# Kernel tuning notes

Hardware: AMD Instinct MI355X
Metric: run time of the kernel (lower is better)

Reference implementation:

```python
import jax, jax.numpy as jnp
import numpy as np

B, N, F = 8, 1024, 256
OUT, REL = 256, 16
NADJ = 7  # ((2 relations + consecutive) * 2 for backward) + self link


def setup_inputs() -> dict:
    key = jax.random.key(0)
    k0, k1, k2, k3, k4 = jax.random.split(key, 5)
    features = jax.random.normal(k0, (B, N, F), dtype=jnp.float32)
    A1 = jax.random.uniform(k1, (B, N, N), dtype=jnp.float32)
    A2 = jax.random.uniform(k2, (B, N, N), dtype=jnp.float32)
    # learned params: one (F+REL, OUT) weight per adjacency matrix, edge embeddings init 'ones', bias (N, OUT)
    W = jax.random.normal(k3, (NADJ, F + REL, OUT), dtype=jnp.float32) * 0.05
    W_edges = jnp.ones((NADJ, REL), dtype=jnp.float32)
    b = jax.random.uniform(k4, (N, OUT), dtype=jnp.float32, minval=-0.05, maxval=0.05)
    return {"features": features, "A1": A1, "A2": A2, "W": W, "W_edges": W_edges, "b": b}


def reference(features, A1, A2, W, W_edges, b):
    # eye = A[0] * zeros(N) + eye(N)  -> batch-broadcast identity [B,N,N]
    eye = jnp.zeros_like(A1) + jnp.eye(N, dtype=A1.dtype)
    # original rolls along axis 0 (batch) of the broadcast identity (faithful replication)
    shifted = jnp.roll(eye, 1, axis=0)
    A_fwd = [A1, A2, shifted]                      # relations + consecutive link
    A_list = A_fwd + [jnp.swapaxes(a, 1, 2) for a in A_fwd]  # backward links
    A_list.append(eye)                             # self links
    A = jnp.stack(A_list, axis=0)                  # [R,B,N,N]

    # concat(features, tile(W_edges[r])) @ W[r] == features @ W[r][:F] + W_edges[r] @ W[r][F:]
    HW = jnp.einsum('bnf,rfo->rbno', features, W[:, :F]) \
         + jnp.einsum('rd,rdo->ro', W_edges, W[:, F:])[:, None, None, :]  # [R,B,N,OUT]
    AHW = jnp.einsum('rbnm,rbmo->rbno', A, HW)     # batched adjacency matmul
    out = jnp.max(AHW, axis=0) + b                 # max-aggregate over relations, add bias
    return out                                     # activation = linear
```

## Files before the change

### kernel.cpp

```cpp
#include <hip/hip_runtime.h>
#include <hip/hip_bf16.h>

#define B_ 8
#define N_ 1024
#define F_ 256
#define OUT_ 256
#define REL_ 16
#define NADJ_ 7

typedef __attribute__((ext_vector_type(8))) _Float16 f16x8;
typedef __attribute__((ext_vector_type(4))) float f32x4;

__device__ __forceinline__ void gll16(const _Float16* g, _Float16* l) {
    __builtin_amdgcn_global_load_lds(
        (const __attribute__((address_space(1))) void*)g,
        (__attribute__((address_space(3))) void*)l, 16, 0, 0);
}

__constant__ const int c_perm[7] = {0, 1, 3, 4, 2, 5, 6};

__global__ __launch_bounds__(256) void convprep_kernel(const float* __restrict__ A1,
                                                       const float* __restrict__ A2,
                                                       const float* __restrict__ W,
                                                       const float* __restrict__ We,
                                                       const float* __restrict__ feat,
                                                       _Float16* __restrict__ Af,
                                                       float* __restrict__ cb,
                                                       _Float16* __restrict__ WTp,
                                                       _Float16* __restrict__ Fe) {
    __shared__ _Float16 T[4096];
    int bid = blockIdx.x, t = threadIdx.x;
    if (bid < 4096) {
        int z = bid >> 8, s = z >> 3, b = z & 7;
        const float* src = (s ? A2 : A1) + (size_t)b * N_ * N_;
        int k0 = (bid & 15) * 64, n0 = ((bid >> 4) & 15) * 64;
        int r = t >> 2, cs = (t & 3) * 16;
        const float* sp = src + (size_t)(k0 + r) * N_ + n0 + cs;
        _Float16 v[16];
#pragma unroll
        for (int j = 0; j < 16; j += 4) {
            float4 f = *(const float4*)(sp + j);
            v[j] = (_Float16)f.x; v[j + 1] = (_Float16)f.y;
            v[j + 2] = (_Float16)f.z; v[j + 3] = (_Float16)f.w;
        }
        const size_t slab = (size_t)8 * N_ * N_;
        {
            _Float16* dst = Af + (size_t)s * slab + (size_t)b * N_ * N_ + (size_t)(k0 + r) * N_ + n0 + cs;
            f16x8 p0 = {v[0], v[1], v[2], v[3], v[4], v[5], v[6], v[7]};
            f16x8 p1 = {v[8], v[9], v[10], v[11], v[12], v[13], v[14], v[15]};
            *(f16x8*)dst = p0;
            *(f16x8*)(dst + 8) = p1;
        }
#pragma unroll
        for (int j = 0; j < 16; ++j) {
            int n = cs + j;
            int sw = ((n ^ (n >> 3)) & 7) << 3;
            T[n * 64 + (r ^ sw)] = v[j];
        }
        __syncthreads();
        {
            int n = t >> 2, i2 = (t & 3) * 16;
            int sw = ((n ^ (n >> 3)) & 7) << 3;
            f16x8 q0 = *(const f16x8*)&T[n * 64 + (i2 ^ sw)];
            f16x8 q1 = *(const f16x8*)&T[n * 64 + ((i2 + 8) ^ sw)];
            _Float16* dt = Af + (size_t)(2 + s) * slab + (size_t)b * N_ * N_ + (size_t)(n0 + n) * N_ + k0 + i2;
            *(f16x8*)dt = q0;
            *(f16x8*)(dt + 8) = q1;
        }
    } else if (bid < 4103) {
        int idx = (bid - 4096) * 256 + t;
        int j = idx / OUT_, o = idx % OUT_;
        int r = c_perm[j];
        const float* Wr = W + (size_t)r * (F_ + REL_) * OUT_;
        float s = 0.f;
#pragma unroll
        for (int d = 0; d < REL_; ++d) s += We[r * REL_ + d] * Wr[(F_ + d) * OUT_ + o];
        cb[idx] = s;
    } else if (bid < 5895) {
        int idx = (bid - 4103) * 256 + t;
        int j = idx >> 16, rem = idx & 65535, o = rem >> 8, f = rem & 255;
        int r = c_perm[j];
        WTp[idx] = (_Float16)W[((size_t)r * (F_ + REL_) + f) * OUT_ + o];
    } else {
        int i = (bid - 5895) * 256 + t;
        size_t base = (size_t)i * 8;
        float4 a = *(const float4*)(feat + base);
        float4 b = *(const float4*)(feat + base + 4);
        f16x8 v = {(_Float16)a.x, (_Float16)a.y, (_Float16)a.z, (_Float16)a.w,
                   (_Float16)b.x, (_Float16)b.y, (_Float16)b.z, (_Float16)b.w};
        *(f16x8*)(Fe + base) = v;
    }
}

__global__ __launch_bounds__(256) void hw7_kernel(const _Float16* __restrict__ Fe,
                                                  const _Float16* __restrict__ WTp,
                                                  const float* __restrict__ cb,
                                                  _Float16* __restrict__ HWT,
                                                  _Float16* __restrict__ HWN) {
    __shared__ _Float16 As[128 * 32];
    __shared__ _Float16 Bs[128 * 32];
    const int z = blockIdx.z, bx = blockIdx.x, by = blockIdx.y;
    const bool tr = (z < 4);
    const _Float16* A  = tr ? (WTp + (size_t)z * 65536) : Fe;
    const _Float16* Bt = tr ? Fe : (WTp + (size_t)z * 65536);
    const int m0 = (tr ? by : bx) * 128;
    const int n0 = (tr ? bx : by) * 128;
    const int tid = threadIdx.x;
    const int wave = tid >> 6, lane = tid & 63, lm = lane & 15, q = lane >> 4;
    const int wr = (wave >> 1) * 64, wc = (wave & 1) * 64;
    const int srow = tid >> 2, sk = (tid & 3) * 8;
    const _Float16* ga0 = A + (size_t)(m0 + srow) * F_ + sk;
    const _Float16* ga1 = ga0 + (size_t)64 * F_;
    const _Float16* gb0 = Bt + (size_t)(n0 + srow) * F_ + sk;
    const _Float16* gb1 = gb0 + (size_t)64 * F_;
    _Float16* la0 = As + tid * 8;
    _Float16* la1 = As + 2048 + tid * 8;
    _Float16* lb0 = Bs + tid * 8;
    _Float16* lb1 = Bs + 2048 + tid * 8;

    f32x4 acc[4][4] = {};
    for (int k0 = 0; k0 < F_; k0 += 32) {
        gll16(ga0 + k0, la0);
        gll16(ga1 + k0, la1);
        gll16(gb0 + k0, lb0);
        gll16(gb1 + k0, lb1);
        __syncthreads();
        f16x8 af[4], bf[4];
#pragma unroll
        for (int i = 0; i < 4; ++i) af[i] = *(const f16x8*)(As + (wr + i * 16 + lm) * 32 + q * 8);
#pragma unroll
        for (int j = 0; j < 4; ++j) bf[j] = *(const f16x8*)(Bs + (wc + j * 16 + lm) * 32 + q * 8);
#pragma unroll
        for (int i = 0; i < 4; ++i)
#pragma unroll
            for (int j = 0; j < 4; ++j)
                acc[i][j] = __builtin_amdgcn_mfma_f32_16x16x32_f16(af[i], bf[j], acc[i][j], 0, 0, 0);
        __syncthreads();
    }
    const float* cbz = cb + (size_t)z * 256;
    if (tr) {
        _Float16* C = HWT + (size_t)z * ((size_t)256 * 8192);
#pragma unroll
        for (int i = 0; i < 4; ++i)
#pragma unroll
            for (int j = 0; j < 4; ++j)
#pragma unroll
                for (int g = 0; g < 4; ++g) {
                    int row = wr + i * 16 + q * 4 + g;
                    int col = wc + j * 16 + lm;
                    float v = acc[i][j][g] + cbz[m0 + row];
                    C[(size_t)(m0 + row) * 8192 + (n0 + col)] = (_Float16)v;
                }
    } else {
        _Float16* C = HWN + (size_t)(z - 4) * ((size_t)8192 * 256);
#pragma unroll
        for (int i = 0; i < 4; ++i)
#pragma unroll
            for (int j = 0; j < 4; ++j)
#pragma unroll
                for (int g = 0; g < 4; ++g) {
                    int row = wr + i * 16 + q * 4 + g;
                    int col = wc + j * 16 + lm;
                    float v = acc[i][j][g] + cbz[n0 + col];
                    C[(size_t)(m0 + row) * 256 + (n0 + col)] = (_Float16)v;
                }
    }
}

__global__ __launch_bounds__(256) void p2_kernel(const _Float16* __restrict__ Af,
                                                 const _Float16* __restrict__ HWT,
                                                 _Float16* __restrict__ AHW) {
    __shared__ _Float16 As[128 * 32];
    __shared__ _Float16 Bs[128 * 32];
    const int d = blockIdx.x;
    const int member = (d >> 3) & 1;
    const int p = (d & 7) | ((d >> 4) << 3);
    const int mt = p & 7, zz = p >> 3;
    const int rr = zz >> 3, b = zz & 7;
    const _Float16* A  = Af + (size_t)rr * (8 * 1048576) + (size_t)b * 1048576;
    const _Float16* Bt = HWT + (size_t)rr * (256 * 8192) + (size_t)b * 1024;
    _Float16* C = AHW + (size_t)rr * (8 * 262144) + (size_t)b * 262144;
    const int m0 = mt * 128, n0 = member * 128;
    const int tid = threadIdx.x;
    const int wave = tid >> 6, lane = tid & 63, lm = lane & 15, q = lane >> 4;
    const int wr = (wave >> 1) * 64, wc = (wave & 1) * 64;
    const int srow = tid >> 2, sk = (tid & 3) * 8;
    const _Float16* ga0 = A + (size_t)(m0 + srow) * N_ + sk;
    const _Float16* ga1 = ga0 + (size_t)64 * N_;
    const _Float16* gb0 = Bt + (size_t)(n0 + srow) * 8192 + sk;
    const _Float16* gb1 = gb0 + (size_t)64 * 8192;
    _Float16* la0 = As + tid * 8;
    _Float16* la1 = As + 2048 + tid * 8;
    _Float16* lb0 = Bs + tid * 8;
    _Float16* lb1 = Bs + 2048 + tid * 8;

    f32x4 acc[4][4] = {};
    for (int k0 = 0; k0 < N_; k0 += 32) {
        gll16(ga0 + k0, la0);
        gll16(ga1 + k0, la1);
        gll16(gb0 + k0, lb0);
        gll16(gb1 + k0, lb1);
        __syncthreads();
        f16x8 af[4], bf[4];
#pragma unroll
        for (int i = 0; i < 4; ++i) af[i] = *(const f16x8*)(As + (wr + i * 16 + lm) * 32 + q * 8);
#pragma unroll
        for (int j = 0; j < 4; ++j) bf[j] = *(const f16x8*)(Bs + (wc + j * 16 + lm) * 32 + q * 8);
#pragma unroll
        for (int i = 0; i < 4; ++i)
#pragma unroll
            for (int j = 0; j < 4; ++j)
                acc[i][j] = __builtin_amdgcn_mfma_f32_16x16x32_f16(af[i], bf[j], acc[i][j], 0, 0, 0);
        __syncthreads();
    }
#pragma unroll
    for (int i = 0; i < 4; ++i)
#pragma unroll
        for (int j = 0; j < 4; ++j)
#pragma unroll
            for (int g = 0; g < 4; ++g) {
                int row = wr + i * 16 + q * 4 + g;
                int col = wc + j * 16 + lm;
                C[(size_t)(m0 + row) * 256 + (n0 + col)] = (_Float16)acc[i][j][g];
            }
}

__global__ __launch_bounds__(256) void max_kernel(const _Float16* __restrict__ AHW,
                                                  const _Float16* __restrict__ HWN,
                                                  const float* __restrict__ bias,
                                                  float* __restrict__ out) {
    size_t i = ((size_t)blockIdx.x * 256 + threadIdx.x) * 8;
    const size_t slab = (size_t)B_ * N_ * OUT_;
    float m[8];
    f16x8 v = *(const f16x8*)(AHW + i);
#pragma unroll
    for (int e = 0; e < 8; ++e) m[e] = (float)v[e];
#pragma unroll
    for (int rr = 1; rr < 4; ++rr) {
        f16x8 w = *(const f16x8*)(AHW + rr * slab + i);
#pragma unroll
        for (int e = 0; e < 8; ++e) m[e] = fmaxf(m[e], (float)w[e]);
    }
#pragma unroll
    for (int j = 0; j < 3; ++j) {
        f16x8 w = *(const f16x8*)(HWN + j * slab + i);
#pragma unroll
        for (int e = 0; e < 8; ++e) m[e] = fmaxf(m[e], (float)w[e]);
    }
    size_t bidx = i & ((size_t)N_ * OUT_ - 1);
    float4 b0 = *(const float4*)(bias + bidx);
    float4 b1 = *(const float4*)(bias + bidx + 4);
    float4 o0 = {m[0] + b0.x, m[1] + b0.y, m[2] + b0.z, m[3] + b0.w};
    float4 o1 = {m[4] + b1.x, m[5] + b1.y, m[6] + b1.z, m[7] + b1.w};
    *(float4*)(out + i) = o0;
    *(float4*)(out + i + 4) = o1;
}

__global__ void cbias_kernel(const float* __restrict__ W, const float* __restrict__ We,
                             float* __restrict__ c) {
    int idx = blockIdx.x * 256 + threadIdx.x;
    if (idx >= NADJ_ * OUT_) return;
    int r = idx / OUT_, o = idx % OUT_;
    const float* Wr = W + (size_t)r * (F_ + REL_) * OUT_;
    float s = 0.f;
#pragma unroll
    for (int d = 0; d < REL_; ++d) s += We[r * REL_ + d] * Wr[(F_ + d) * OUT_ + o];
    c[idx] = s;
}

__global__ __launch_bounds__(256) void hw_kernel(const float* __restrict__ feat,
                                                 const float* __restrict__ W,
                                                 const float* __restrict__ cb,
                                                 _Float16* __restrict__ HWb) {
    __shared__ _Float16 As[64][32];
    __shared__ _Float16 Bs[64][32];
    const int mt = blockIdx.x, ct = blockIdx.y;
    const int tid = threadIdx.x, wave = tid >> 6, lane = tid & 63;
    const int r = (ct * 64) / OUT_;
    const int o0 = (ct * 64) % OUT_;
    const float* Bg = W + (size_t)r * (F_ + REL_) * OUT_ + o0;
    const int m0 = mt * 64;
    const int lm = lane & 15, q = lane >> 4;
    f32x4 acc[4] = {};
    for (int k0 = 0; k0 < F_; k0 += 32) {
        {
            int seg = (tid & 3) * 8, m = tid >> 2;
            const float* src = feat + (size_t)(m0 + m) * F_ + k0 + seg;
#pragma unroll
            for (int j = 0; j < 8; ++j) As[m][seg + j] = (_Float16)src[j];
        }
        {
            int kk = tid >> 3, ns = (tid & 7) * 8;
            const float* src = Bg + (size_t)(k0 + kk) * OUT_ + ns;
#pragma unroll
            for (int j = 0; j < 8; ++j) Bs[ns + j][kk] = (_Float16)src[j];
        }
        __syncthreads();
        f16x8 a = *(const f16x8*)&As[wave * 16 + lm][q * 8];
#pragma unroll
        for (int c4 = 0; c4 < 4; ++c4) {
            f16x8 b = *(const f16x8*)&Bs[c4 * 16 + lm][q * 8];
            acc[c4] = __builtin_amdgcn_mfma_f32_16x16x32_f16(a, b, acc[c4], 0, 0, 0);
        }
        __syncthreads();
    }
#pragma unroll
    for (int c4 = 0; c4 < 4; ++c4)
#pragma unroll
        for (int g = 0; g < 4; ++g) {
            int row = wave * 16 + (lane >> 4) * 4 + g;
            int col = c4 * 16 + lm;
            float v = acc[c4][g] + cb[r * OUT_ + o0 + col];
            HWb[((size_t)r * B_ * N_ + m0 + row) * OUT_ + o0 + col] = (_Float16)v;
        }
}

__global__ __launch_bounds__(256) void agg_kernel(const float* __restrict__ A1,
                                                  const float* __restrict__ A2,
                                                  const _Float16* __restrict__ HWb,
                                                  const float* __restrict__ bias,
                                                  float* __restrict__ out) {
    __shared__ _Float16 As[64][32];
    __shared__ _Float16 Bs[64][32];
    const int b = blockIdx.z, nt = blockIdx.y, ot = blockIdx.x;
    const int tid = threadIdx.x, wave = tid >> 6, lane = tid & 63;
    const int n0 = nt * 64, o0 = ot * 64;
    const int lm = lane & 15, q = lane >> 4;
    const size_t rstride = (size_t)B_ * N_ * OUT_;
    f32x4 mx[4];
#pragma unroll
    for (int i = 0; i < 4; ++i) mx[i] = f32x4{-1e30f, -1e30f, -1e30f, -1e30f};
#pragma unroll 1
    for (int rr = 0; rr < 4; ++rr) {
        const float* Ag = ((rr & 1) ? A2 : A1) + (size_t)b * N_ * N_;
        const bool tr = (rr >= 2);
        const int r = (rr < 2) ? rr : rr + 1;
        const _Float16* Bg = HWb + (size_t)r * rstride + (size_t)b * N_ * OUT_ + o0;
        f32x4 acc[4] = {};
        for (int k0 = 0; k0 < N_; k0 += 32) {
            if (!tr) {
                int seg = (tid & 3) * 8, m = tid >> 2;
                const float* src = Ag + (size_t)(n0 + m) * N_ + k0 + seg;
#pragma unroll
                for (int j = 0; j < 8; ++j) As[m][seg + j] = (_Float16)src[j];
            } else {
                int kk = tid >> 3, ms = (tid & 7) * 8;
                const float* src = Ag + (size_t)(k0 + kk) * N_ + n0 + ms;
#pragma unroll
                for (int j = 0; j < 8; ++j) As[ms + j][kk] = (_Float16)src[j];
            }
            {
                int kk = tid >> 3, ns = (tid & 7) * 8;
                const _Float16* src = Bg + (size_t)(k0 + kk) * OUT_ + ns;
#pragma unroll
                for (int j = 0; j < 8; ++j) Bs[ns + j][kk] = src[j];
            }
            __syncthreads();
            f16x8 a = *(const f16x8*)&As[wave * 16 + lm][q * 8];
#pragma unroll
            for (int c4 = 0; c4 < 4; ++c4) {
                f16x8 bb = *(const f16x8*)&Bs[c4 * 16 + lm][q * 8];
                acc[c4] = __builtin_amdgcn_mfma_f32_16x16x32_f16(a, bb, acc[c4], 0, 0, 0);
            }
            __syncthreads();
        }
#pragma unroll
        for (int c4 = 0; c4 < 4; ++c4)
#pragma unroll
            for (int g = 0; g < 4; ++g) mx[c4][g] = fmaxf(mx[c4][g], acc[c4][g]);
    }
#pragma unroll
    for (int c4 = 0; c4 < 4; ++c4)
#pragma unroll
        for (int g = 0; g < 4; ++g) {
            int row = wave * 16 + (lane >> 4) * 4 + g;
            int col = c4 * 16 + lm;
            size_t pos = ((size_t)b * N_ + n0 + row) * OUT_ + o0 + col;
            float v = mx[c4][g];
            v = fmaxf(v, (float)HWb[2 * rstride + pos]);
            v = fmaxf(v, (float)HWb[5 * rstride + pos]);
            v = fmaxf(v, (float)HWb[6 * rstride + pos]);
            out[pos] = v + bias[((size_t)(n0 + row)) * OUT_ + o0 + col];
        }
}

extern "C" void kernel_launch(void* const* d_in, const int* in_sizes, int n_in,
                              void* d_out, int out_size, void* d_ws, size_t ws_size,
                              hipStream_t stream) {
    const float* feat = (const float*)d_in[0];
    const float* A1   = (const float*)d_in[1];
    const float* A2   = (const float*)d_in[2];
    const float* W    = (const float*)d_in[3];
    const float* We   = (const float*)d_in[4];
    const float* bias = (const float*)d_in[5];
    float* out = (float*)d_out;

    const size_t OFF_CB   = 0;
    const size_t OFF_WT   = 8192;
    const size_t OFF_FE   = 1048576;
    const size_t OFF_AF   = 5242880;
    const size_t OFF_HWT  = 72351744;
    const size_t OFF_HWN  = 89128960;
    const size_t OFF_AHW  = 101711872;
    const size_t WS_NEEDED = 118489088;

    if (ws_size >= WS_NEEDED) {
        float*    cbp = (float*)((char*)d_ws + OFF_CB);
        _Float16* WTp = (_Float16*)((char*)d_ws + OFF_WT);
        _Float16* Fe  = (_Float16*)((char*)d_ws + OFF_FE);
        _Float16* Af  = (_Float16*)((char*)d_ws + OFF_AF);
        _Float16* HWT = (_Float16*)((char*)d_ws + OFF_HWT);
        _Float16* HWN = (_Float16*)((char*)d_ws + OFF_HWN);
        _Float16* AHW = (_Float16*)((char*)d_ws + OFF_AHW);

        convprep_kernel<<<6919, 256, 0, stream>>>(A1, A2, W, We, feat, Af, cbp, WTp, Fe);
        hw7_kernel<<<dim3(64, 2, 7), 256, 0, stream>>>(Fe, WTp, cbp, HWT, HWN);
        p2_kernel<<<512, 256, 0, stream>>>(Af, HWT, AHW);
        max_kernel<<<1024, 256, 0, stream>>>(AHW, HWN, bias, out);
    } else {
        float* cb = (float*)d_ws;
        _Float16* HWb = (_Float16*)((char*)d_ws + 8192);
        cbias_kernel<<<7, 256, 0, stream>>>(W, We, cb);
        hw_kernel<<<dim3(128, 28), 256, 0, stream>>>(feat, W, cb, HWb);
        agg_kernel<<<dim3(4, 16, 8), 256, 0, stream>>>(A1, A2, HWb, bias, out);
    }
}
```

Baseline: 179.1 us.

## Fuse adjacency conversion with HW GEMM and fold relation max into aggregation

The pipeline goes from four kernels to three. The small prep work (bias constants, weight transpose, feature cast) now runs first. The A1/A2 fp16 conversion and transpose share one launch with the HW GEMM tiles, so the two can overlap. The aggregation GEMM loops over the four adjacency relations inside each block and keeps a running max in registers, then folds in the three HWN slabs and the bias before writing fp32 output. This removes the fp16 AHW intermediate and its round trip through memory, but the aggregation grid drops to 256 blocks with narrower 64-column tiles, which may underfill the GPU.

Measured after the change: 197.9 us. 1.1x slower.

```diff
diff --git a/kernel.cpp b/kernel.cpp
--- a/kernel.cpp
+++ b/kernel.cpp
@@ -19,22 +19,123 @@
 
 __constant__ const int c_perm[7] = {0, 1, 3, 4, 2, 5, 6};
 
-__global__ __launch_bounds__(256) void convprep_kernel(const float* __restrict__ A1,
-                                                       const float* __restrict__ A2,
-                                                       const float* __restrict__ W,
-                                                       const float* __restrict__ We,
-                                                       const float* __restrict__ feat,
-                                                       _Float16* __restrict__ Af,
-                                                       float* __restrict__ cb,
-                                                       _Float16* __restrict__ WTp,
-                                                       _Float16* __restrict__ Fe) {
-    __shared__ _Float16 T[4096];
-    int bid = blockIdx.x, t = threadIdx.x;
-    if (bid < 4096) {
-        int z = bid >> 8, s = z >> 3, b = z & 7;
+__global__ __launch_bounds__(256) void prep_kernel(const float* __restrict__ W,
+                                                   const float* __restrict__ We,
+                                                   const float* __restrict__ feat,
+                                                   float* __restrict__ cb,
+                                                   _Float16* __restrict__ WTp,
+                                                   _Float16* __restrict__ Fe) {
+    int bid = blockIdx.x, tid = threadIdx.x;
+    if (bid < 7) {
+        int idx = bid * 256 + tid;
+        int j = idx / OUT_, o = idx % OUT_;
+        int r = c_perm[j];
+        const float* Wr = W + (size_t)r * (F_ + REL_) * OUT_;
+        float s = 0.f;
+#pragma unroll
+        for (int d = 0; d < REL_; ++d) s += We[r * REL_ + d] * Wr[(F_ + d) * OUT_ + o];
+        cb[idx] = s;
+    } else if (bid < 1799) {
+        int idx = (bid - 7) * 256 + tid;
+        int j = idx >> 16, rem = idx & 65535, o = rem >> 8, f = rem & 255;
+        int r = c_perm[j];
+        WTp[idx] = (_Float16)W[((size_t)r * (F_ + REL_) + f) * OUT_ + o];
+    } else {
+        int i = (bid - 1799) * 256 + tid;
+        size_t base = (size_t)i * 8;
+        float4 a = *(const float4*)(feat + base);
+        float4 b = *(const float4*)(feat + base + 4);
+        f16x8 v = {(_Float16)a.x, (_Float16)a.y, (_Float16)a.z, (_Float16)a.w,
+                   (_Float16)b.x, (_Float16)b.y, (_Float16)b.z, (_Float16)b.w};
+        *(f16x8*)(Fe + base) = v;
+    }
+}
+
+__global__ __launch_bounds__(256) void convhw_kernel(const float* __restrict__ A1,
+                                                     const float* __restrict__ A2,
+                                                     const _Float16* __restrict__ Fe,
+                                                     const _Float16* __restrict__ WTp,
+                                                     const float* __restrict__ cb,
+                                                     _Float16* __restrict__ Af,
+                                                     _Float16* __restrict__ HWT,
+                                                     _Float16* __restrict__ HWN) {
+    __shared__ _Float16 S[8192];
+    const int bid = blockIdx.x, tid = threadIdx.x;
+    if (bid < 896) {
+        const int z = bid / 128, rem = bid % 128, bx = rem & 63, by = rem >> 6;
+        const bool tr = (z < 4);
+        const _Float16* A  = tr ? (WTp + (size_t)z * 65536) : Fe;
+        const _Float16* Bt = tr ? Fe : (WTp + (size_t)z * 65536);
+        const int m0 = (tr ? by : bx) * 128;
+        const int n0 = (tr ? bx : by) * 128;
+        _Float16* As = S;
+        _Float16* Bs = S + 4096;
+        const int wave = tid >> 6, lane = tid & 63, lm = lane & 15, q = lane >> 4;
+        const int wr = (wave >> 1) * 64, wc = (wave & 1) * 64;
+        const int srow = tid >> 2, sk = (tid & 3) * 8;
+        const _Float16* ga0 = A + (size_t)(m0 + srow) * F_ + sk;
+        const _Float16* ga1 = ga0 + (size_t)64 * F_;
+        const _Float16* gb0 = Bt + (size_t)(n0 + srow) * F_ + sk;
+        const _Float16* gb1 = gb0 + (size_t)64 * F_;
+        _Float16* la0 = As + tid * 8;
+        _Float16* la1 = As + 2048 + tid * 8;
+        _Float16* lb0 = Bs + tid * 8;
+        _Float16* lb1 = Bs + 2048 + tid * 8;
+
+        f32x4 acc[4][4] = {};
+        for (int k0 = 0; k0 < F_; k0 += 32) {
+            gll16(ga0 + k0, la0);
+            gll16(ga1 + k0, la1);
+            gll16(gb0 + k0, lb0);
+            gll16(gb1 + k0, lb1);
+            __syncthreads();
+            f16x8 af[4], bf[4];
+#pragma unroll
+            for (int i = 0; i < 4; ++i) af[i] = *(const f16x8*)(As + (wr + i * 16 + lm) * 32 + q * 8);
+#pragma unroll
+            for (int j = 0; j < 4; ++j) bf[j] = *(const f16x8*)(Bs + (wc + j * 16 + lm) * 32 + q * 8);
+#pragma unroll
+            for (int i = 0; i < 4; ++i)
+#pragma unroll
+                for (int j = 0; j < 4; ++j)
+                    acc[i][j] = __builtin_amdgcn_mfma_f32_16x16x32_f16(af[i], bf[j], acc[i][j], 0, 0, 0);
+            __syncthreads();
+        }
+        const float* cbz = cb + (size_t)z * 256;
+        if (tr) {
+            _Float16* C = HWT + (size_t)z * ((size_t)256 * 8192);
+#pragma unroll
+            for (int i = 0; i < 4; ++i)
+#pragma unroll
+                for (int j = 0; j < 4; ++j)
+#pragma unroll
+                    for (int g = 0; g < 4; ++g) {
+                        int row = wr + i * 16 + q * 4 + g;
+                        int col = wc + j * 16 + lm;
+                        float v = acc[i][j][g] + cbz[m0 + row];
+                        C[(size_t)(m0 + row) * 8192 + (n0 + col)] = (_Float16)v;
+                    }
+        } else {
+            _Float16* C = HWN + (size_t)(z - 4) * ((size_t)8192 * 256);
+#pragma unroll
+            for (int i = 0; i < 4; ++i)
+#pragma unroll
+                for (int j = 0; j < 4; ++j)
+#pragma unroll
+                    for (int g = 0; g < 4; ++g) {
+                        int row = wr + i * 16 + q * 4 + g;
+                        int col = wc + j * 16 + lm;
+                        float v = acc[i][j][g] + cbz[n0 + col];
+                        C[(size_t)(m0 + row) * 256 + (n0 + col)] = (_Float16)v;
+                    }
+        }
+    } else {
+        _Float16* T = S;
+        const int cbid = bid - 896;
+        int z = cbid >> 8, s = z >> 3, b = z & 7;
         const float* src = (s ? A2 : A1) + (size_t)b * N_ * N_;
-        int k0 = (bid & 15) * 64, n0 = ((bid >> 4) & 15) * 64;
-        int r = t >> 2, cs = (t & 3) * 16;
+        int k0 = (cbid & 15) * 64, n0 = ((cbid >> 4) & 15) * 64;
+        int r = tid >> 2, cs = (tid & 3) * 16;
         const float* sp = src + (size_t)(k0 + r) * N_ + n0 + cs;
         _Float16 v[16];
 #pragma unroll
@@ -59,7 +160,7 @@
         }
         __syncthreads();
         {
-            int n = t >> 2, i2 = (t & 3) * 16;
+            int n = tid >> 2, i2 = (tid & 3) * 16;
             int sw = ((n ^ (n >> 3)) & 7) << 3;
             f16x8 q0 = *(const f16x8*)&T[n * 64 + (i2 ^ sw)];
             f16x8 q1 = *(const f16x8*)&T[n * 64 + ((i2 + 8) ^ sw)];
@@ -67,193 +168,81 @@
             *(f16x8*)dt = q0;
             *(f16x8*)(dt + 8) = q1;
         }
-    } else if (bid < 4103) {
-        int idx = (bid - 4096) * 256 + t;
-        int j = idx / OUT_, o = idx % OUT_;
-        int r = c_perm[j];
-        const float* Wr = W + (size_t)r * (F_ + REL_) * OUT_;
-        float s = 0.f;
-#pragma unroll
-        for (int d = 0; d < REL_; ++d) s += We[r * REL_ + d] * Wr[(F_ + d) * OUT_ + o];
-        cb[idx] = s;
-    } else if (bid < 5895) {
-        int idx = (bid - 4103) * 256 + t;
-        int j = idx >> 16, rem = idx & 65535, o = rem >> 8, f = rem & 255;
-        int r = c_perm[j];
-        WTp[idx] = (_Float16)W[((size_t)r * (F_ + REL_) + f) * OUT_ + o];
-    } else {
-        int i = (bid - 5895) * 256 + t;
-        size_t base = (size_t)i * 8;
-        float4 a = *(const float4*)(feat + base);
-        float4 b = *(const float4*)(feat + base + 4);
-        f16x8 v = {(_Float16)a.x, (_Float16)a.y, (_Float16)a.z, (_Float16)a.w,
-                   (_Float16)b.x, (_Float16)b.y, (_Float16)b.z, (_Float16)b.w};
-        *(f16x8*)(Fe + base) = v;
-    }
-}
-
-__global__ __launch_bounds__(256) void hw7_kernel(const _Float16* __restrict__ Fe,
-                                                  const _Float16* __restrict__ WTp,
-                                                  const float* __restrict__ cb,
-                                                  _Float16* __restrict__ HWT,
-                                                  _Float16* __restrict__ HWN) {
+    }
+}
+
+__global__ __launch_bounds__(256) void p2max_kernel(const _Float16* __restrict__ Af,
+                                                    const _Float16* __restrict__ HWT,
+                                                    const _Float16* __restrict__ HWN,
+                                                    const float* __restrict__ bias,
+                                                    float* __restrict__ out) {
     __shared__ _Float16 As[128 * 32];
-    __shared__ _Float16 Bs[128 * 32];
-    const int z = blockIdx.z, bx = blockIdx.x, by = blockIdx.y;
-    const bool tr = (z < 4);
-    const _Float16* A  = tr ? (WTp + (size_t)z * 65536) : Fe;
-    const _Float16* Bt = tr ? Fe : (WTp + (size_t)z * 65536);
-    const int m0 = (tr ? by : bx) * 128;
-    const int n0 = (tr ? bx : by) * 128;
+    __shared__ _Float16 Bs[64 * 32];
+    const int d = blockIdx.x;
+    const int b = d & 7, ot = (d >> 3) & 3, nt = d >> 5;
+    const int n0 = nt * 128, o0 = ot * 64;
     const int tid = threadIdx.x;
     const int wave = tid >> 6, lane = tid & 63, lm = lane & 15, q = lane >> 4;
-    const int wr = (wave >> 1) * 64, wc = (wave & 1) * 64;
+    const int wr = (wave >> 1) * 64, wc = (wave & 1) * 32;
     const int srow = tid >> 2, sk = (tid & 3) * 8;
-    const _Float16* ga0 = A + (size_t)(m0 + srow) * F_ + sk;
-    const _Float16* ga1 = ga0 + (size_t)64 * F_;
-    const _Float16* gb0 = Bt + (size_t)(n0 + srow) * F_ + sk;
-    const _Float16* gb1 = gb0 + (size_t)64 * F_;
     _Float16* la0 = As + tid * 8;
     _Float16* la1 = As + 2048 + tid * 8;
     _Float16* lb0 = Bs + tid * 8;
-    _Float16* lb1 = Bs + 2048 + tid * 8;
-
-    f32x4 acc[4][4] = {};
-    for (int k0 = 0; k0 < F_; k0 += 32) {
-        gll16(ga0 + k0, la0);
-        gll16(ga1 + k0, la1);
-        gll16(gb0 + k0, lb0);
-        gll16(gb1 + k0, lb1);
-        __syncthreads();
-        f16x8 af[4], bf[4];
-#pragma unroll
-        for (int i = 0; i < 4; ++i) af[i] = *(const f16x8*)(As + (wr + i * 16 + lm) * 32 + q * 8);
-#pragma unroll
-        for (int j = 0; j < 4; ++j) bf[j] = *(const f16x8*)(Bs + (wc + j * 16 + lm) * 32 + q * 8);
+
+    f32x4 mx[4][2];
+#pragma unroll
+    for (int i = 0; i < 4; ++i)
+#pragma unroll
+        for (int j = 0; j < 2; ++j) mx[i][j] = f32x4{-3e38f, -3e38f, -3e38f, -3e38f};
+
+#pragma unroll 1
+    for (int rr = 0; rr < 4; ++rr) {
+        const _Float16* ga0 = Af + (size_t)rr * (8 * 1048576) + (size_t)b * 1048576
+                              + (size_t)(n0 + srow) * N_ + sk;
+        const _Float16* ga1 = ga0 + (size_t)64 * N_;
+        const _Float16* gb0 = HWT + (size_t)rr * (256 * 8192)
+                              + (size_t)(o0 + srow) * 8192 + (size_t)b * 1024 + sk;
+        f32x4 acc[4][2] = {};
+        for (int k0 = 0; k0 < N_; k0 += 32) {
+            gll16(ga0 + k0, la0);
+            gll16(ga1 + k0, la1);
+            gll16(gb0 + k0, lb0);
+            __syncthreads();
+            f16x8 af[4], bf[2];
+#pragma unroll
+            for (int i = 0; i < 4; ++i) af[i] = *(const f16x8*)(As + (wr + i * 16 + lm) * 32 + q * 8);
+#pragma unroll
+            for (int j = 0; j < 2; ++j) bf[j] = *(const f16x8*)(Bs + (wc + j * 16 + lm) * 32 + q * 8);
+#pragma unroll
+            for (int i = 0; i < 4; ++i)
+#pragma unroll
+                for (int j = 0; j < 2; ++j)
+                    acc[i][j] = __builtin_amdgcn_mfma_f32_16x16x32_f16(af[i], bf[j], acc[i][j], 0, 0, 0);
+            __syncthreads();
+        }
 #pragma unroll
         for (int i = 0; i < 4; ++i)
 #pragma unroll
-            for (int j = 0; j < 4; ++j)
-                acc[i][j] = __builtin_amdgcn_mfma_f32_16x16x32_f16(af[i], bf[j], acc[i][j], 0, 0, 0);
-        __syncthreads();
-    }
-    const float* cbz = cb + (size_t)z * 256;
-    if (tr) {
-        _Float16* C = HWT + (size_t)z * ((size_t)256 * 8192);
-#pragma unroll
-        for (int i = 0; i < 4; ++i)
-#pragma unroll
-            for (int j = 0; j < 4; ++j)
-#pragma unroll
-                for (int g = 0; g < 4; ++g) {
-                    int row = wr + i * 16 + q * 4 + g;
-                    int col = wc + j * 16 + lm;
-                    float v = acc[i][j][g] + cbz[m0 + row];
-                    C[(size_t)(m0 + row) * 8192 + (n0 + col)] = (_Float16)v;
-                }
-    } else {
-        _Float16* C = HWN + (size_t)(z - 4) * ((size_t)8192 * 256);
-#pragma unroll
-        for (int i = 0; i < 4; ++i)
-#pragma unroll
-            for (int j = 0; j < 4; ++j)
-#pragma unroll
-                for (int g = 0; g < 4; ++g) {
-                    int row = wr + i * 16 + q * 4 + g;
-                    int col = wc + j * 16 + lm;
-                    float v = acc[i][j][g] + cbz[n0 + col];
-                    C[(size_t)(m0 + row) * 256 + (n0 + col)] = (_Float16)v;
-                }
-    }
-}
-
-__global__ __launch_bounds__(256) void p2_kernel(const _Float16* __restrict__ Af,
-                                                 const _Float16* __restrict__ HWT,
-                                                 _Float16* __restrict__ AHW) {
-    __shared__ _Float16 As[128 * 32];
-    __shared__ _Float16 Bs[128 * 32];
-    const int d = blockIdx.x;
-    const int member = (d >> 3) & 1;
-    const int p = (d & 7) | ((d >> 4) << 3);
-    const int mt = p & 7, zz = p >> 3;
-    const int rr = zz >> 3, b = zz & 7;
-    const _Float16* A  = Af + (size_t)rr * (8 * 1048576) + (size_t)b * 1048576;
-    const _Float16* Bt = HWT + (size_t)rr * (256 * 8192) + (size_t)b * 1024;
-    _Float16* C = AHW + (size_t)rr * (8 * 262144) + (size_t)b * 262144;
-    const int m0 = mt * 128, n0 = member * 128;
-    const int tid = threadIdx.x;
-    const int wave = tid >> 6, lane = tid & 63, lm = lane & 15, q = lane >> 4;
-    const int wr = (wave >> 1) * 64, wc = (wave & 1) * 64;
-    const int srow = tid >> 2, sk = (tid & 3) * 8;
-    const _Float16* ga0 = A + (size_t)(m0 + srow) * N_ + sk;
-    const _Float16* ga1 = ga0 + (size_t)64 * N_;
-    const _Float16* gb0 = Bt + (size_t)(n0 + srow) * 8192 + sk;
-    const _Float16* gb1 = gb0 + (size_t)64 * 8192;
-    _Float16* la0 = As + tid * 8;
-    _Float16* la1 = As + 2048 + tid * 8;
-    _Float16* lb0 = Bs + tid * 8;
-    _Float16* lb1 = Bs + 2048 + tid * 8;
-
-    f32x4 acc[4][4] = {};
-    for (int k0 = 0; k0 < N_; k0 += 32) {
-        gll16(ga0 + k0, la0);
-        gll16(ga1 + k0, la1);
-        gll16(gb0 + k0, lb0);
-        gll16(gb1 + k0, lb1);
-        __syncthreads();
-        f16x8 af[4], bf[4];
-#pragma unroll
-        for (int i = 0; i < 4; ++i) af[i] = *(const f16x8*)(As + (wr + i * 16 + lm) * 32 + q * 8);
-#pragma unroll
-        for (int j = 0; j < 4; ++j) bf[j] = *(const f16x8*)(Bs + (wc + j * 16 + lm) * 32 + q * 8);
-#pragma unroll
-        for (int i = 0; i < 4; ++i)
-#pragma unroll
-            for (int j = 0; j < 4; ++j)
-                acc[i][j] = __builtin_amdgcn_mfma_f32_16x16x32_f16(af[i], bf[j], acc[i][j], 0, 0, 0);
-        __syncthreads();
-    }
+            for (int j = 0; j < 2; ++j)
+#pragma unroll
+                for (int g = 0; g < 4; ++g) mx[i][j][g] = fmaxf(mx[i][j][g], acc[i][j][g]);
+    }
+    const size_t slab = (size_t)B_ * N_ * OUT_;
 #pragma unroll
     for (int i = 0; i < 4; ++i)
 #pragma unroll
-        for (int j = 0; j < 4; ++j)
+        for (int j = 0; j < 2; ++j)
 #pragma unroll
             for (int g = 0; g < 4; ++g) {
                 int row = wr + i * 16 + q * 4 + g;
                 int col = wc + j * 16 + lm;
-                C[(size_t)(m0 + row) * 256 + (n0 + col)] = (_Float16)acc[i][j][g];
+                size_t pos = ((size_t)b * N_ + n0 + row) * OUT_ + o0 + col;
+                float v = mx[i][j][g];
+                v = fmaxf(v, (float)HWN[pos]);
+                v = fmaxf(v, (float)HWN[slab + pos]);
+                v = fmaxf(v, (float)HWN[2 * slab + pos]);
+                out[pos] = v + bias[(size_t)(n0 + row) * OUT_ + o0 + col];
             }
-}
-
-__global__ __launch_bounds__(256) void max_kernel(const _Float16* __restrict__ AHW,
-                                                  const _Float16* __restrict__ HWN,
-                                                  const float* __restrict__ bias,
-                                                  float* __restrict__ out) {
-    size_t i = ((size_t)blockIdx.x * 256 + threadIdx.x) * 8;
-    const size_t slab = (size_t)B_ * N_ * OUT_;
-    float m[8];
-    f16x8 v = *(const f16x8*)(AHW + i);
-#pragma unroll
-    for (int e = 0; e < 8; ++e) m[e] = (float)v[e];
-#pragma unroll
-    for (int rr = 1; rr < 4; ++rr) {
-        f16x8 w = *(const f16x8*)(AHW + rr * slab + i);
-#pragma unroll
-        for (int e = 0; e < 8; ++e) m[e] = fmaxf(m[e], (float)w[e]);
-    }
-#pragma unroll
-    for (int j = 0; j < 3; ++j) {
-        f16x8 w = *(const f16x8*)(HWN + j * slab + i);
-#pragma unroll
-        for (int e = 0; e < 8; ++e) m[e] = fmaxf(m[e], (float)w[e]);
-    }
-    size_t bidx = i & ((size_t)N_ * OUT_ - 1);
-    float4 b0 = *(const float4*)(bias + bidx);
-    float4 b1 = *(const float4*)(bias + bidx + 4);
-    float4 o0 = {m[0] + b0.x, m[1] + b0.y, m[2] + b0.z, m[3] + b0.w};
-    float4 o1 = {m[4] + b1.x, m[5] + b1.y, m[6] + b1.z, m[7] + b1.w};
-    *(float4*)(out + i) = o0;
-    *(float4*)(out + i + 4) = o1;
 }
 
 __global__ void cbias_kernel(const float* __restrict__ W, const float* __restrict__ We,
@@ -401,8 +390,7 @@
     const size_t OFF_AF   = 5242880;
     const size_t OFF_HWT  = 72351744;
     const size_t OFF_HWN  = 89128960;
-    const size_t OFF_AHW  = 101711872;
-    const size_t WS_NEEDED = 118489088;
+    const size_t WS_NEEDED = 101711872;
 
     if (ws_size >= WS_NEEDED) {
         float*    cbp = (float*)((char*)d_ws + OFF_CB);
@@ -411,12 +399,10 @@
         _Float16* Af  = (_Float16*)((char*)d_ws + OFF_AF);
         _Float16* HWT = (_Float16*)((char*)d_ws + OFF_HWT);
         _Float16* HWN = (_Float16*)((char*)d_ws + OFF_HWN);
-        _Float16* AHW = (_Float16*)((char*)d_ws + OFF_AHW);
-
-        convprep_kernel<<<6919, 256, 0, stream>>>(A1, A2, W, We, feat, Af, cbp, WTp, Fe);
-        hw7_kernel<<<dim3(64, 2, 7), 256, 0, stream>>>(Fe, WTp, cbp, HWT, HWN);
-        p2_kernel<<<512, 256, 0, stream>>>(Af, HWT, AHW);
-        max_kernel<<<1024, 256, 0, stream>>>(AHW, HWN, bias, out);
+
+        prep_kernel<<<2823, 256, 0, stream>>>(W, We, feat, cbp, WTp, Fe);
+        convhw_kernel<<<4992, 256, 0, stream>>>(A1, A2, Fe, WTp, cbp, Af, HWT, HWN);
+        p2max_kernel<<<256, 256, 0, stream>>>(Af, HWT, HWN, bias, out);
     } else {
         float* cb = (float*)d_ws;
         _Float16* HWb = (_Float16*)((char*)d_ws + 8192);
```

## Overlap adjacency conversion with HW GEMM in one fused launch

Applied to the files above, without the earlier changes.

Splits the small weight/feature prep into its own kernel and merges the large fp32-to-fp16 adjacency conversion and transpose into the same launch as the HW projection GEMM. The compute-bound GEMM blocks and the bandwidth-bound conversion blocks can then run concurrently on the GPU instead of one after the other. The cost is a shared LDS allocation sized for the larger branch, which may lower occupancy for the conversion blocks, and the GEMM now has to wait for the prep kernel.

New measurement: 176.7 us. Within noise of the previous version (-1.4%).

```diff
diff --git a/kernel.cpp b/kernel.cpp
--- a/kernel.cpp
+++ b/kernel.cpp
@@ -19,22 +19,123 @@
 
 __constant__ const int c_perm[7] = {0, 1, 3, 4, 2, 5, 6};
 
-__global__ __launch_bounds__(256) void convprep_kernel(const float* __restrict__ A1,
-                                                       const float* __restrict__ A2,
-                                                       const float* __restrict__ W,
-                                                       const float* __restrict__ We,
-                                                       const float* __restrict__ feat,
-                                                       _Float16* __restrict__ Af,
-                                                       float* __restrict__ cb,
-                                                       _Float16* __restrict__ WTp,
-                                                       _Float16* __restrict__ Fe) {
-    __shared__ _Float16 T[4096];
-    int bid = blockIdx.x, t = threadIdx.x;
-    if (bid < 4096) {
-        int z = bid >> 8, s = z >> 3, b = z & 7;
+__global__ __launch_bounds__(256) void prep_kernel(const float* __restrict__ W,
+                                                   const float* __restrict__ We,
+                                                   const float* __restrict__ feat,
+                                                   float* __restrict__ cb,
+                                                   _Float16* __restrict__ WTp,
+                                                   _Float16* __restrict__ Fe) {
+    int bid = blockIdx.x, tid = threadIdx.x;
+    if (bid < 7) {
+        int idx = bid * 256 + tid;
+        int j = idx / OUT_, o = idx % OUT_;
+        int r = c_perm[j];
+        const float* Wr = W + (size_t)r * (F_ + REL_) * OUT_;
+        float s = 0.f;
+#pragma unroll
+        for (int d = 0; d < REL_; ++d) s += We[r * REL_ + d] * Wr[(F_ + d) * OUT_ + o];
+        cb[idx] = s;
+    } else if (bid < 1799) {
+        int idx = (bid - 7) * 256 + tid;
+        int j = idx >> 16, rem = idx & 65535, o = rem >> 8, f = rem & 255;
+        int r = c_perm[j];
+        WTp[idx] = (_Float16)W[((size_t)r * (F_ + REL_) + f) * OUT_ + o];
+    } else {
+        int i = (bid - 1799) * 256 + tid;
+        size_t base = (size_t)i * 8;
+        float4 a = *(const float4*)(feat + base);
+        float4 b = *(const float4*)(feat + base + 4);
+        f16x8 v = {(_Float16)a.x, (_Float16)a.y, (_Float16)a.z, (_Float16)a.w,
+                   (_Float16)b.x, (_Float16)b.y, (_Float16)b.z, (_Float16)b.w};
+        *(f16x8*)(Fe + base) = v;
+    }
+}
+
+__global__ __launch_bounds__(256) void convhw_kernel(const float* __restrict__ A1,
+                                                     const float* __restrict__ A2,
+                                                     const _Float16* __restrict__ Fe,
+                                                     const _Float16* __restrict__ WTp,
+                                                     const float* __restrict__ cb,
+                                                     _Float16* __restrict__ Af,
+                                                     _Float16* __restrict__ HWT,
+                                                     _Float16* __restrict__ HWN) {
+    __shared__ _Float16 S[8192];
+    const int bid = blockIdx.x, tid = threadIdx.x;
+    if (bid < 896) {
+        const int z = bid / 128, rem = bid % 128, bx = rem & 63, by = rem >> 6;
+        const bool tr = (z < 4);
+        const _Float16* A  = tr ? (WTp + (size_t)z * 65536) : Fe;
+        const _Float16* Bt = tr ? Fe : (WTp + (size_t)z * 65536);
+        const int m0 = (tr ? by : bx) * 128;
+        const int n0 = (tr ? bx : by) * 128;
+        _Float16* As = S;
+        _Float16* Bs = S + 4096;
+        const int wave = tid >> 6, lane = tid & 63, lm = lane & 15, q = lane >> 4;
+        const int wr = (wave >> 1) * 64, wc = (wave & 1) * 64;
+        const int srow = tid >> 2, sk = (tid & 3) * 8;
+        const _Float16* ga0 = A + (size_t)(m0 + srow) * F_ + sk;
+        const _Float16* ga1 = ga0 + (size_t)64 * F_;
+        const _Float16* gb0 = Bt + (size_t)(n0 + srow) * F_ + sk;
+        const _Float16* gb1 = gb0 + (size_t)64 * F_;
+        _Float16* la0 = As + tid * 8;
+        _Float16* la1 = As + 2048 + tid * 8;
+        _Float16* lb0 = Bs + tid * 8;
+        _Float16* lb1 = Bs + 2048 + tid * 8;
+
+        f32x4 acc[4][4] = {};
+        for (int k0 = 0; k0 < F_; k0 += 32) {
+            gll16(ga0 + k0, la0);
+            gll16(ga1 + k0, la1);
+            gll16(gb0 + k0, lb0);
+            gll16(gb1 + k0, lb1);
+            __syncthreads();
+            f16x8 af[4], bf[4];
+#pragma unroll
+            for (int i = 0; i < 4; ++i) af[i] = *(const f16x8*)(As + (wr + i * 16 + lm) * 32 + q * 8);
+#pragma unroll
+            for (int j = 0; j < 4; ++j) bf[j] = *(const f16x8*)(Bs + (wc + j * 16 + lm) * 32 + q * 8);
+#pragma unroll
+            for (int i = 0; i < 4; ++i)
+#pragma unroll
+                for (int j = 0; j < 4; ++j)
+                    acc[i][j] = __builtin_amdgcn_mfma_f32_16x16x32_f16(af[i], bf[j], acc[i][j], 0, 0, 0);
+            __syncthreads();
+        }
+        const float* cbz = cb + (size_t)z * 256;
+        if (tr) {
+            _Float16* C = HWT + (size_t)z * ((size_t)256 * 8192);
+#pragma unroll
+            for (int i = 0; i < 4; ++i)
+#pragma unroll
+                for (int j = 0; j < 4; ++j)
+#pragma unroll
+                    for (int g = 0; g < 4; ++g) {
+                        int row = wr + i * 16 + q * 4 + g;
+                        int col = wc + j * 16 + lm;
+                        float v = acc[i][j][g] + cbz[m0 + row];
+                        C[(size_t)(m0 + row) * 8192 + (n0 + col)] = (_Float16)v;
+                    }
+        } else {
+            _Float16* C = HWN + (size_t)(z - 4) * ((size_t)8192 * 256);
+#pragma unroll
+            for (int i = 0; i < 4; ++i)
+#pragma unroll
+                for (int j = 0; j < 4; ++j)
+#pragma unroll
+                    for (int g = 0; g < 4; ++g) {
+                        int row = wr + i * 16 + q * 4 + g;
+                        int col = wc + j * 16 + lm;
+                        float v = acc[i][j][g] + cbz[n0 + col];
+                        C[(size_t)(m0 + row) * 256 + (n0 + col)] = (_Float16)v;
+                    }
+        }
+    } else {
+        _Float16* T = S;
+        const int cbid = bid - 896;
+        int z = cbid >> 8, s = z >> 3, b = z & 7;
         const float* src = (s ? A2 : A1) + (size_t)b * N_ * N_;
-        int k0 = (bid & 15) * 64, n0 = ((bid >> 4) & 15) * 64;
-        int r = t >> 2, cs = (t & 3) * 16;
+        int k0 = (cbid & 15) * 64, n0 = ((cbid >> 4) & 15) * 64;
+        int r = tid >> 2, cs = (tid & 3) * 16;
         const float* sp = src + (size_t)(k0 + r) * N_ + n0 + cs;
         _Float16 v[16];
 #pragma unroll
@@ -59,7 +160,7 @@
         }
         __syncthreads();
         {
-            int n = t >> 2, i2 = (t & 3) * 16;
+            int n = tid >> 2, i2 = (tid & 3) * 16;
             int sw = ((n ^ (n >> 3)) & 7) << 3;
             f16x8 q0 = *(const f16x8*)&T[n * 64 + (i2 ^ sw)];
             f16x8 q1 = *(const f16x8*)&T[n * 64 + ((i2 + 8) ^ sw)];
@@ -67,103 +168,6 @@
             *(f16x8*)dt = q0;
             *(f16x8*)(dt + 8) = q1;
         }
-    } else if (bid < 4103) {
-        int idx = (bid - 4096) * 256 + t;
-        int j = idx / OUT_, o = idx % OUT_;
-        int r = c_perm[j];
-        const float* Wr = W + (size_t)r * (F_ + REL_) * OUT_;
-        float s = 0.f;
-#pragma unroll
-        for (int d = 0; d < REL_; ++d) s += We[r * REL_ + d] * Wr[(F_ + d) * OUT_ + o];
-        cb[idx] = s;
-    } else if (bid < 5895) {
-        int idx = (bid - 4103) * 256 + t;
-        int j = idx >> 16, rem = idx & 65535, o = rem >> 8, f = rem & 255;
-        int r = c_perm[j];
-        WTp[idx] = (_Float16)W[((size_t)r * (F_ + REL_) + f) * OUT_ + o];
-    } else {
-        int i = (bid - 5895) * 256 + t;
-        size_t base = (size_t)i * 8;
-        float4 a = *(const float4*)(feat + base);
-        float4 b = *(const float4*)(feat + base + 4);
-        f16x8 v = {(_Float16)a.x, (_Float16)a.y, (_Float16)a.z, (_Float16)a.w,
-                   (_Float16)b.x, (_Float16)b.y, (_Float16)b.z, (_Float16)b.w};
-        *(f16x8*)(Fe + base) = v;
-    }
-}
-
-__global__ __launch_bounds__(256) void hw7_kernel(const _Float16* __restrict__ Fe,
-                                                  const _Float16* __restrict__ WTp,
-                                                  const float* __restrict__ cb,
-                                                  _Float16* __restrict__ HWT,
-                                                  _Float16* __restrict__ HWN) {
-    __shared__ _Float16 As[128 * 32];
-    __shared__ _Float16 Bs[128 * 32];
-    const int z = blockIdx.z, bx = blockIdx.x, by = blockIdx.y;
-    const bool tr = (z < 4);
-    const _Float16* A  = tr ? (WTp + (size_t)z * 65536) : Fe;
-    const _Float16* Bt = tr ? Fe : (WTp + (size_t)z * 65536);
-    const int m0 = (tr ? by : bx) * 128;
-    const int n0 = (tr ? bx : by) * 128;
-    const int tid = threadIdx.x;
-    const int wave = tid >> 6, lane = tid & 63, lm = lane & 15, q = lane >> 4;
-    const int wr = (wave >> 1) * 64, wc = (wave & 1) * 64;
-    const int srow = tid >> 2, sk = (tid & 3) * 8;
-    const _Float16* ga0 = A + (size_t)(m0 + srow) * F_ + sk;
-    const _Float16* ga1 = ga0 + (size_t)64 * F_;
-    const _Float16* gb0 = Bt + (size_t)(n0 + srow) * F_ + sk;
-    const _Float16* gb1 = gb0 + (size_t)64 * F_;
-    _Float16* la0 = As + tid * 8;
-    _Float16* la1 = As + 2048 + tid * 8;
-    _Float16* lb0 = Bs + tid * 8;
-    _Float16* lb1 = Bs + 2048 + tid * 8;
-
-    f32x4 acc[4][4] = {};
-    for (int k0 = 0; k0 < F_; k0 += 32) {
-        gll16(ga0 + k0, la0);
-        gll16(ga1 + k0, la1);
-        gll16(gb0 + k0, lb0);
-        gll16(gb1 + k0, lb1);
-        __syncthreads();
-        f16x8 af[4], bf[4];
-#pragma unroll
-        for (int i = 0; i < 4; ++i) af[i] = *(const f16x8*)(As + (wr + i * 16 + lm) * 32 + q * 8);
-#pragma unroll
-        for (int j = 0; j < 4; ++j) bf[j] = *(const f16x8*)(Bs + (wc + j * 16 + lm) * 32 + q * 8);
-#pragma unroll
-        for (int i = 0; i < 4; ++i)
-#pragma unroll
-            for (int j = 0; j < 4; ++j)
-                acc[i][j] = __builtin_amdgcn_mfma_f32_16x16x32_f16(af[i], bf[j], acc[i][j], 0, 0, 0);
-        __syncthreads();
-    }
-    const float* cbz = cb + (size_t)z * 256;
-    if (tr) {
-        _Float16* C = HWT + (size_t)z * ((size_t)256 * 8192);
-#pragma unroll
-        for (int i = 0; i < 4; ++i)
-#pragma unroll
-            for (int j = 0; j < 4; ++j)
-#pragma unroll
-                for (int g = 0; g < 4; ++g) {
-                    int row = wr + i * 16 + q * 4 + g;
-                    int col = wc + j * 16 + lm;
-                    float v = acc[i][j][g] + cbz[m0 + row];
-                    C[(size_t)(m0 + row) * 8192 + (n0 + col)] = (_Float16)v;
-                }
-    } else {
-        _Float16* C = HWN + (size_t)(z - 4) * ((size_t)8192 * 256);
-#pragma unroll
-        for (int i = 0; i < 4; ++i)
-#pragma unroll
-            for (int j = 0; j < 4; ++j)
-#pragma unroll
-                for (int g = 0; g < 4; ++g) {
-                    int row = wr + i * 16 + q * 4 + g;
-                    int col = wc + j * 16 + lm;
-                    float v = acc[i][j][g] + cbz[n0 + col];
-                    C[(size_t)(m0 + row) * 256 + (n0 + col)] = (_Float16)v;
-                }
     }
 }
 
@@ -413,8 +417,8 @@
         _Float16* HWN = (_Float16*)((char*)d_ws + OFF_HWN);
         _Float16* AHW = (_Float16*)((char*)d_ws + OFF_AHW);
 
-        convprep_kernel<<<6919, 256, 0, stream>>>(A1, A2, W, We, feat, Af, cbp, WTp, Fe);
-        hw7_kernel<<<dim3(64, 2, 7), 256, 0, stream>>>(Fe, WTp, cbp, HWT, HWN);
+        prep_kernel<<<2823, 256, 0, stream>>>(W, We, feat, cbp, WTp, Fe);
+        convhw_kernel<<<4992, 256, 0, stream>>>(A1, A2, Fe, WTp, cbp, Af, HWT, HWN);
         p2_kernel<<<512, 256, 0, stream>>>(Af, HWT, AHW);
         max_kernel<<<1024, 256, 0, stream>>>(AHW, HWN, bias, out);
     } else {
```
